# Kernel optimization log

Measured on AMD Instinct MI355X. Metric: run time of the kernel, lower is better.

## Reference

```python
import jax, jax.numpy as jnp
import numpy as np

TOP_K = 2

def setup_inputs() -> dict:
    key = jax.random.key(0)
    k0, k1, k2 = jax.random.split(key, 3)
    N, D, E = 32768, 1024, 8  # tokens, in_dim, expert_num
    x = jax.random.normal(k0, (N, D), dtype=jnp.float32)
    W1 = jax.random.normal(k1, (D // 2, D), dtype=jnp.float32) * (1.0 / np.sqrt(D))
    b1 = jnp.zeros((D // 2,), dtype=jnp.float32)
    W2 = jax.random.normal(k2, (E, D // 2), dtype=jnp.float32) * (1.0 / np.sqrt(D // 2))
    b2 = jnp.zeros((E,), dtype=jnp.float32)
    return {"x": x, "W1": W1, "b1": b1, "W2": W2, "b2": b2}

def reference(x, W1, b1, W2, b2):
    E = W2.shape[0]
    # gate: two stacked Linears (no nonlinearity between, as in source)
    h = x @ W1.T + b1                      # [N, D/2]
    router_logits = h @ W2.T + b2          # [N, E]
    router_probs = jax.nn.softmax(router_logits, axis=-1)
    router_weights, top_k_indices = jax.lax.top_k(router_probs, TOP_K)  # [N, K]
    router_weights = router_weights / jnp.sum(router_weights, axis=-1, keepdims=True)
    expert_masks = jax.nn.one_hot(top_k_indices, E, dtype=jnp.int32)   # [N, K, E]
    expert_masks = jnp.transpose(expert_masks, (2, 1, 0))              # [E, K, N]
    return (router_logits, router_weights, top_k_indices, expert_masks)
```

## Files before the change

kernel.cpp:

```cpp
#include <hip/hip_runtime.h>
#include <math.h>


#define N_TOK 32768
#define D_IN  1024
#define D_H   512
#define N_EXP 8

#define BM      128
#define BK      16
#define THREADS 512
#define NKT     (D_IN / BK)
#define WSLOTS  (NKT * 1024)

typedef _Float16 f16;
typedef __attribute__((ext_vector_type(4)))  _Float16 f16x4;
typedef __attribute__((ext_vector_type(8)))  _Float16 f16x8;
typedef __attribute__((ext_vector_type(16))) float    f32x16;

#define MFMA(a, b, c) __builtin_amdgcn_mfma_f32_32x32x16_f16((a), (b), (c), 0, 0, 0)

__global__ void split_w1(const float* __restrict__ W1,
                         f16* __restrict__ wsH, f16* __restrict__ wsL) {
    const int s = blockIdx.x * 256 + threadIdx.x;
    const int kt  = s >> 10;
    const int ctg = (s >> 6) & 15;
    const int l   = s & 63;
    const int n   = ctg * 32 + (l & 31);
    const int k   = kt * BK + (l >> 5) * 8;
    const float* src = &W1[(size_t)n * D_IN + k];
    float4 a0 = *(const float4*)src;
    float4 a1 = *(const float4*)(src + 4);
    f16x8 hi, lo;
#pragma unroll
    for (int j = 0; j < 4; ++j) {
        float v0 = ((const float*)&a0)[j];
        float v1 = ((const float*)&a1)[j];
        _Float16 h0 = (_Float16)v0, h1 = (_Float16)v1;
        hi[j] = h0;     hi[j + 4] = h1;
        lo[j] = (_Float16)(v0 - (float)h0);
        lo[j + 4] = (_Float16)(v1 - (float)h1);
    }
    *(f16x8*)&wsH[(size_t)s * 8] = hi;
    *(f16x8*)&wsL[(size_t)s * 8] = lo;
}

__global__ __launch_bounds__(THREADS, 1)
void moe_router_mfma(const float* __restrict__ x,
                     const f16* __restrict__ wH,
                     const f16* __restrict__ wL,
                     const float* __restrict__ b1,
                     const float* __restrict__ W2,
                     const float* __restrict__ b2,
                     float* __restrict__ out)
{
    __shared__ __align__(16) f16   AS[2 * 2 * 2048];
    __shared__ __align__(16) float h_s[32 * 512];
    __shared__ __align__(16) float W2s[N_EXP * D_H];
    __shared__ __align__(16) float b1s[D_H];
    __shared__ float b2s[N_EXP];

    const int t    = threadIdx.x;
    const int w    = t >> 6;
    const int lane = t & 63;
    const int m0   = blockIdx.x * BM;

    f32x16 a0c0 = {}, a0c1 = {}, a1c0 = {}, a1c1 = {};
    f32x16 a2c0 = {}, a2c1 = {}, a3c0 = {}, a3c1 = {};

    const int fA   = t >> 1;
    const int qA   = t & 1;
    const int rowA = (fA >> 6) * 32 + (fA & 31);
    const int kA   = ((fA >> 5) & 1) * 8 + qA * 4;
    const float* xsrc = x + (size_t)(m0 + rowA) * D_IN + kA;
    const int aDst = fA * 8 + qA * 4;

    const size_t bOff0 = (size_t)(2 * w + 0) * 512 + (size_t)lane * 8;
    const size_t bOff1 = (size_t)(2 * w + 1) * 512 + (size_t)lane * 8;

    auto stageAwrite = [&](const float4& xv, int buf) {
        f16x4 hi, lo;
        float v[4] = {xv.x, xv.y, xv.z, xv.w};
#pragma unroll
        for (int j = 0; j < 4; ++j) {
            _Float16 h = (_Float16)v[j];
            hi[j] = h;
            lo[j] = (_Float16)(v[j] - (float)h);
        }
        *(f16x4*)&AS[(buf * 2 + 0) * 2048 + aDst] = hi;
        *(f16x4*)&AS[(buf * 2 + 1) * 2048 + aDst] = lo;
    };

    f16x8 Bh0A = *(const f16x8*)(wH + bOff0);
    f16x8 Bh1A = *(const f16x8*)(wH + bOff1);
    f16x8 Bl0A = *(const f16x8*)(wL + bOff0);
    f16x8 Bl1A = *(const f16x8*)(wL + bOff1);
    f16x8 Bh0B, Bh1B, Bl0B, Bl1B;
    {
        float4 xv = *(const float4*)xsrc;
        stageAwrite(xv, 0);
    }
    __syncthreads();

#define BODY(BUF, KT, BH0, BH1, BL0, BL1, NH0, NH1, NL0, NL1) do {             \
        float4 xnxt = {0.f, 0.f, 0.f, 0.f};                                    \
        if ((KT) + 1 < NKT) {                                                  \
            const size_t nb = (size_t)((KT) + 1) * 8192;                       \
            NH0 = *(const f16x8*)(wH + nb + bOff0);                            \
            NH1 = *(const f16x8*)(wH + nb + bOff1);                            \
            NL0 = *(const f16x8*)(wL + nb + bOff0);                            \
            NL1 = *(const f16x8*)(wL + nb + bOff1);                            \
            xnxt = *(const float4*)(xsrc + (size_t)((KT) + 1) * BK);           \
        }                                                                      \
        const f16* ah = &AS[((BUF) * 2 + 0) * 2048];                           \
        const f16* al = &AS[((BUF) * 2 + 1) * 2048];                           \
        f16x8 ah0 = *(const f16x8*)&ah[(0 * 64 + lane) * 8];                   \
        f16x8 al0 = *(const f16x8*)&al[(0 * 64 + lane) * 8];                   \
        f16x8 ah1 = *(const f16x8*)&ah[(1 * 64 + lane) * 8];                   \
        f16x8 al1 = *(const f16x8*)&al[(1 * 64 + lane) * 8];                   \
        f16x8 ah2 = *(const f16x8*)&ah[(2 * 64 + lane) * 8];                   \
        f16x8 al2 = *(const f16x8*)&al[(2 * 64 + lane) * 8];                   \
        f16x8 ah3 = *(const f16x8*)&ah[(3 * 64 + lane) * 8];                   \
        f16x8 al3 = *(const f16x8*)&al[(3 * 64 + lane) * 8];                   \
        __builtin_amdgcn_s_setprio(1);                                         \
        a0c0 = MFMA(ah0, BH0, a0c0); a0c0 = MFMA(al0, BH0, a0c0);              \
        a0c0 = MFMA(ah0, BL0, a0c0);                                           \
        a1c0 = MFMA(ah1, BH0, a1c0); a1c0 = MFMA(al1, BH0, a1c0);              \
        a1c0 = MFMA(ah1, BL0, a1c0);                                           \
        a2c0 = MFMA(ah2, BH0, a2c0); a2c0 = MFMA(al2, BH0, a2c0);              \
        a2c0 = MFMA(ah2, BL0, a2c0);                                           \
        a3c0 = MFMA(ah3, BH0, a3c0); a3c0 = MFMA(al3, BH0, a3c0);              \
        a3c0 = MFMA(ah3, BL0, a3c0);                                           \
        __builtin_amdgcn_s_setprio(0);                                         \
        __builtin_amdgcn_s_barrier();                                          \
        __builtin_amdgcn_s_setprio(1);                                         \
        a0c1 = MFMA(ah0, BH1, a0c1); a0c1 = MFMA(al0, BH1, a0c1);              \
        a0c1 = MFMA(ah0, BL1, a0c1);                                           \
        a1c1 = MFMA(ah1, BH1, a1c1); a1c1 = MFMA(al1, BH1, a1c1);              \
        a1c1 = MFMA(ah1, BL1, a1c1);                                           \
        a2c1 = MFMA(ah2, BH1, a2c1); a2c1 = MFMA(al2, BH1, a2c1);              \
        a2c1 = MFMA(ah2, BL1, a2c1);                                           \
        a3c1 = MFMA(ah3, BH1, a3c1); a3c1 = MFMA(al3, BH1, a3c1);              \
        a3c1 = MFMA(ah3, BL1, a3c1);                                           \
        __builtin_amdgcn_s_setprio(0);                                         \
        if ((KT) + 1 < NKT) stageAwrite(xnxt, (BUF) ^ 1);                      \
        __syncthreads();                                                       \
    } while (0)

    for (int kt = 0; kt < NKT; kt += 2) {
        BODY(0, kt,     Bh0A, Bh1A, Bl0A, Bl1A, Bh0B, Bh1B, Bl0B, Bl1B);
        BODY(1, kt + 1, Bh0B, Bh1B, Bl0B, Bl1B, Bh0A, Bh1A, Bl0A, Bl1A);
    }
#undef BODY

    ((float4*)W2s)[t * 2]     = ((const float4*)W2)[t * 2];
    ((float4*)W2s)[t * 2 + 1] = ((const float4*)W2)[t * 2 + 1];
    if (t < D_H / 4) ((float4*)b1s)[t] = ((const float4*)b1)[t];
    if (t < N_EXP) b2s[t] = b2[t];
    __syncthreads();

    const int n0  = w * 64 + (lane & 31);
    const int n1  = n0 + 32;
    const float bn0 = b1s[n0];
    const float bn1 = b1s[n1];

    float* out_logits = out;
    float* out_w      = out + (size_t)N_TOK * N_EXP;
    float* out_i      = out_w + (size_t)N_TOK * 2;
    float* out_m      = out_i + (size_t)N_TOK * 2;

    auto reduce_rows = [&](int rt) {
#pragma unroll
        for (int rr2 = 0; rr2 < 4; ++rr2) {
            const int rl   = w * 4 + rr2;
            const int grow = m0 + rt * 32 + rl;
            float4 ha = *(const float4*)&h_s[rl * 512 + lane * 4];
            float4 hb = *(const float4*)&h_s[rl * 512 + 256 + lane * 4];
            float v1 = -3.4e38f, v2 = -3.4e38f;
            int   i1 = 0, i2 = 0;
            float pls[8];
#pragma unroll
            for (int e = 0; e < N_EXP; ++e) {
                float4 wa = *(const float4*)&W2s[e * D_H + lane * 4];
                float4 wb = *(const float4*)&W2s[e * D_H + 256 + lane * 4];
                float s = ha.x * wa.x;
                s = fmaf(ha.y, wa.y, s);
                s = fmaf(ha.z, wa.z, s);
                s = fmaf(ha.w, wa.w, s);
                s = fmaf(hb.x, wb.x, s);
                s = fmaf(hb.y, wb.y, s);
                s = fmaf(hb.z, wb.z, s);
                s = fmaf(hb.w, wb.w, s);
#pragma unroll
                for (int off = 1; off < 64; off <<= 1)
                    s += __shfl_xor(s, off);
                s += b2s[e];
                pls[e] = s;
                if (s > v1)      { v2 = v1; i2 = i1; v1 = s; i1 = e; }
                else if (s > v2) { v2 = s;  i2 = e; }
            }
            const float rr   = expf(v2 - v1);
            const float wden = 1.f / (1.f + rr);
            if (lane == 0) {
                float4 lo4 = {pls[0], pls[1], pls[2], pls[3]};
                float4 hi4 = {pls[4], pls[5], pls[6], pls[7]};
                *(float4*)&out_logits[(size_t)grow * N_EXP]     = lo4;
                *(float4*)&out_logits[(size_t)grow * N_EXP + 4] = hi4;
                float2 wv = {wden, rr * wden};
                *(float2*)&out_w[(size_t)grow * 2] = wv;
                float2 iv = {(float)i1, (float)i2};
                *(float2*)&out_i[(size_t)grow * 2] = iv;
            }
            if (lane < 16) {
                const int e   = lane >> 1;
                const int kk  = lane & 1;
                const int sel = kk ? i2 : i1;
                out_m[((size_t)(e * 2 + kk)) * N_TOK + grow] = (sel == e) ? 1.0f : 0.0f;
            }
        }
    };

#define DO_GROUP(AC0, AC1, RT) do {                                            \
        _Pragma("unroll")                                                      \
        for (int rr = 0; rr < 16; ++rr) {                                      \
            const int rl = (rr & 3) + 8 * (rr >> 2) + 4 * (lane >> 5);         \
            h_s[rl * 512 + n0] = AC0[rr] + bn0;                                \
            h_s[rl * 512 + n1] = AC1[rr] + bn1;                                \
        }                                                                      \
        __syncthreads();                                                       \
        reduce_rows(RT);                                                       \
        __syncthreads();                                                       \
    } while (0)

    DO_GROUP(a0c0, a0c1, 0);
    DO_GROUP(a1c0, a1c1, 1);
    DO_GROUP(a2c0, a2c1, 2);
    DO_GROUP(a3c0, a3c1, 3);
#undef DO_GROUP
}

extern "C" void kernel_launch(void* const* d_in, const int* in_sizes, int n_in,
                              void* d_out, int out_size, void* d_ws, size_t ws_size,
                              hipStream_t stream) {
    const float* x  = (const float*)d_in[0];
    const float* W1 = (const float*)d_in[1];
    const float* b1 = (const float*)d_in[2];
    const float* W2 = (const float*)d_in[3];
    const float* b2 = (const float*)d_in[4];
    float* out = (float*)d_out;

    f16* wsH = (f16*)d_ws;
    f16* wsL = wsH + (size_t)WSLOTS * 8;

    split_w1<<<WSLOTS / 256, 256, 0, stream>>>(W1, wsH, wsL);
    moe_router_mfma<<<N_TOK / BM, THREADS, 0, stream>>>(x, wsH, wsL, b1, W2, b2, out);
}
```

Baseline: 130.6 us.

## Double K-step per barrier, interleave MFMA order, alias LDS buffers

```diff
diff --git a/kernel.cpp b/kernel.cpp
--- a/kernel.cpp
+++ b/kernel.cpp
@@ -8,10 +8,9 @@
 #define N_EXP 8
 
 #define BM      128
-#define BK      16
 #define THREADS 512
-#define NKT     (D_IN / BK)
-#define WSLOTS  (NKT * 1024)
+#define NKT2    32
+#define WSLOTS  (64 * 1024)
 
 typedef _Float16 f16;
 typedef __attribute__((ext_vector_type(4)))  _Float16 f16x4;
@@ -27,7 +26,7 @@
     const int ctg = (s >> 6) & 15;
     const int l   = s & 63;
     const int n   = ctg * 32 + (l & 31);
-    const int k   = kt * BK + (l >> 5) * 8;
+    const int k   = kt * 16 + (l >> 5) * 8;
     const float* src = &W1[(size_t)n * D_IN + k];
     float4 a0 = *(const float4*)src;
     float4 a1 = *(const float4*)(src + 4);
@@ -54,11 +53,13 @@
                      const float* __restrict__ b2,
                      float* __restrict__ out)
 {
-    __shared__ __align__(16) f16   AS[2 * 2 * 2048];
-    __shared__ __align__(16) float h_s[32 * 512];
+    __shared__ __align__(16) unsigned char SMEM[65536];
     __shared__ __align__(16) float W2s[N_EXP * D_H];
     __shared__ __align__(16) float b1s[D_H];
     __shared__ float b2s[N_EXP];
+
+    f16*   AS  = (f16*)SMEM;
+    float* h_s = (float*)SMEM;
 
     const int t    = threadIdx.x;
     const int w    = t >> 6;
@@ -72,13 +73,17 @@
     const int qA   = t & 1;
     const int rowA = (fA >> 6) * 32 + (fA & 31);
     const int kA   = ((fA >> 5) & 1) * 8 + qA * 4;
-    const float* xsrc = x + (size_t)(m0 + rowA) * D_IN + kA;
+    const unsigned xOff = (unsigned)(m0 + rowA) * D_IN + kA;
     const int aDst = fA * 8 + qA * 4;
 
-    const size_t bOff0 = (size_t)(2 * w + 0) * 512 + (size_t)lane * 8;
-    const size_t bOff1 = (size_t)(2 * w + 1) * 512 + (size_t)lane * 8;
-
-    auto stageAwrite = [&](const float4& xv, int buf) {
+    const unsigned bO0 = (unsigned)(2 * w + 0) * 512 + (unsigned)lane * 8;
+    const unsigned bO1 = bO0 + 512;
+    const int aO0 = ((0 * 64) + lane) * 8;
+    const int aO1 = ((1 * 64) + lane) * 8;
+    const int aO2 = ((2 * 64) + lane) * 8;
+    const int aO3 = ((3 * 64) + lane) * 8;
+
+    auto stageAwrite = [&](const float4& xv, int buf, int sub) {
         f16x4 hi, lo;
         float v[4] = {xv.x, xv.y, xv.z, xv.w};
 #pragma unroll
@@ -87,69 +92,130 @@
             hi[j] = h;
             lo[j] = (_Float16)(v[j] - (float)h);
         }
-        *(f16x4*)&AS[(buf * 2 + 0) * 2048 + aDst] = hi;
-        *(f16x4*)&AS[(buf * 2 + 1) * 2048 + aDst] = lo;
+        *(f16x4*)&AS[(buf * 2 + 0) * 4096 + sub * 2048 + aDst] = hi;
+        *(f16x4*)&AS[(buf * 2 + 1) * 4096 + sub * 2048 + aDst] = lo;
     };
 
-    f16x8 Bh0A = *(const f16x8*)(wH + bOff0);
-    f16x8 Bh1A = *(const f16x8*)(wH + bOff1);
-    f16x8 Bl0A = *(const f16x8*)(wL + bOff0);
-    f16x8 Bl1A = *(const f16x8*)(wL + bOff1);
-    f16x8 Bh0B, Bh1B, Bl0B, Bl1B;
-    {
-        float4 xv = *(const float4*)xsrc;
-        stageAwrite(xv, 0);
-    }
+    stageAwrite(*(const float4*)(x + xOff), 0, 0);
+    stageAwrite(*(const float4*)(x + (xOff + 16u)), 0, 1);
+    f16x8 AH00 = *(const f16x8*)(wH + bO0);
+    f16x8 AH01 = *(const f16x8*)(wH + bO1);
+    f16x8 AH10 = *(const f16x8*)(wH + (8192u + bO0));
+    f16x8 AH11 = *(const f16x8*)(wH + (8192u + bO1));
+    f16x8 AL00 = *(const f16x8*)(wL + bO0);
+    f16x8 AL01 = *(const f16x8*)(wL + bO1);
+    f16x8 AL10 = *(const f16x8*)(wL + (8192u + bO0));
+    f16x8 AL11 = *(const f16x8*)(wL + (8192u + bO1));
+    f16x8 BH00, BH01, BH10, BH11, BL00, BL01, BL10, BL11;
     __syncthreads();
 
-#define BODY(BUF, KT, BH0, BH1, BL0, BL1, NH0, NH1, NL0, NL1) do {             \
-        float4 xnxt = {0.f, 0.f, 0.f, 0.f};                                    \
-        if ((KT) + 1 < NKT) {                                                  \
-            const size_t nb = (size_t)((KT) + 1) * 8192;                       \
-            NH0 = *(const f16x8*)(wH + nb + bOff0);                            \
-            NH1 = *(const f16x8*)(wH + nb + bOff1);                            \
-            NL0 = *(const f16x8*)(wL + nb + bOff0);                            \
-            NL1 = *(const f16x8*)(wL + nb + bOff1);                            \
-            xnxt = *(const float4*)(xsrc + (size_t)((KT) + 1) * BK);           \
-        }                                                                      \
-        const f16* ah = &AS[((BUF) * 2 + 0) * 2048];                           \
-        const f16* al = &AS[((BUF) * 2 + 1) * 2048];                           \
-        f16x8 ah0 = *(const f16x8*)&ah[(0 * 64 + lane) * 8];                   \
-        f16x8 al0 = *(const f16x8*)&al[(0 * 64 + lane) * 8];                   \
-        f16x8 ah1 = *(const f16x8*)&ah[(1 * 64 + lane) * 8];                   \
-        f16x8 al1 = *(const f16x8*)&al[(1 * 64 + lane) * 8];                   \
-        f16x8 ah2 = *(const f16x8*)&ah[(2 * 64 + lane) * 8];                   \
-        f16x8 al2 = *(const f16x8*)&al[(2 * 64 + lane) * 8];                   \
-        f16x8 ah3 = *(const f16x8*)&ah[(3 * 64 + lane) * 8];                   \
-        f16x8 al3 = *(const f16x8*)&al[(3 * 64 + lane) * 8];                   \
-        __builtin_amdgcn_s_setprio(1);                                         \
-        a0c0 = MFMA(ah0, BH0, a0c0); a0c0 = MFMA(al0, BH0, a0c0);              \
-        a0c0 = MFMA(ah0, BL0, a0c0);                                           \
-        a1c0 = MFMA(ah1, BH0, a1c0); a1c0 = MFMA(al1, BH0, a1c0);              \
-        a1c0 = MFMA(ah1, BL0, a1c0);                                           \
-        a2c0 = MFMA(ah2, BH0, a2c0); a2c0 = MFMA(al2, BH0, a2c0);              \
-        a2c0 = MFMA(ah2, BL0, a2c0);                                           \
-        a3c0 = MFMA(ah3, BH0, a3c0); a3c0 = MFMA(al3, BH0, a3c0);              \
-        a3c0 = MFMA(ah3, BL0, a3c0);                                           \
-        __builtin_amdgcn_s_setprio(0);                                         \
-        __builtin_amdgcn_s_barrier();                                          \
-        __builtin_amdgcn_s_setprio(1);                                         \
-        a0c1 = MFMA(ah0, BH1, a0c1); a0c1 = MFMA(al0, BH1, a0c1);              \
-        a0c1 = MFMA(ah0, BL1, a0c1);                                           \
-        a1c1 = MFMA(ah1, BH1, a1c1); a1c1 = MFMA(al1, BH1, a1c1);              \
-        a1c1 = MFMA(ah1, BL1, a1c1);                                           \
-        a2c1 = MFMA(ah2, BH1, a2c1); a2c1 = MFMA(al2, BH1, a2c1);              \
-        a2c1 = MFMA(ah2, BL1, a2c1);                                           \
-        a3c1 = MFMA(ah3, BH1, a3c1); a3c1 = MFMA(al3, BH1, a3c1);              \
-        a3c1 = MFMA(ah3, BL1, a3c1);                                           \
-        __builtin_amdgcn_s_setprio(0);                                         \
-        if ((KT) + 1 < NKT) stageAwrite(xnxt, (BUF) ^ 1);                      \
+#define BODY(BUF, KTT, CH00, CH01, CH10, CH11, CL00, CL01, CL10, CL11,         \
+                       NH00, NH01, NH10, NH11, NL00, NL01, NL10, NL11)         \
+    do {                                                                       \
+        float4 xn0 = {0.f, 0.f, 0.f, 0.f}, xn1 = {0.f, 0.f, 0.f, 0.f};         \
+        const bool more = (KTT) + 1 < NKT2;                                    \
+        if (more) {                                                            \
+            const unsigned nk = (unsigned)(2 * (KTT) + 2) * 8192u;             \
+            NH00 = *(const f16x8*)(wH + (nk + bO0));                           \
+            NH01 = *(const f16x8*)(wH + (nk + bO1));                           \
+            NH10 = *(const f16x8*)(wH + (nk + 8192u + bO0));                   \
+            NH11 = *(const f16x8*)(wH + (nk + 8192u + bO1));                   \
+            xn0 = *(const float4*)(x + (xOff + (unsigned)((KTT) + 1) * 32u));  \
+            xn1 = *(const float4*)(x + (xOff + (unsigned)((KTT) + 1) * 32u + 16u)); \
+        }                                                                      \
+        const int hiP = ((BUF) * 2 + 0) * 4096;                                \
+        const int loP = ((BUF) * 2 + 1) * 4096;                                \
+        {                                                 \
+            f16x8 ah0 = *(const f16x8*)&AS[hiP + aO0];                         \
+            f16x8 ah1 = *(const f16x8*)&AS[hiP + aO1];                         \
+            f16x8 ah2 = *(const f16x8*)&AS[hiP + aO2];                         \
+            f16x8 ah3 = *(const f16x8*)&AS[hiP + aO3];                         \
+            f16x8 al0 = *(const f16x8*)&AS[loP + aO0];                         \
+            f16x8 al1 = *(const f16x8*)&AS[loP + aO1];                         \
+            f16x8 al2 = *(const f16x8*)&AS[loP + aO2];                         \
+            f16x8 al3 = *(const f16x8*)&AS[loP + aO3];                         \
+            __builtin_amdgcn_s_setprio(1);                                     \
+            a0c0 = MFMA(ah0, CH00, a0c0);                                      \
+            a1c0 = MFMA(ah1, CH00, a1c0);                                      \
+            a2c0 = MFMA(ah2, CH00, a2c0);                                      \
+            a3c0 = MFMA(ah3, CH00, a3c0);                                      \
+            a0c1 = MFMA(ah0, CH01, a0c1);                                      \
+            a1c1 = MFMA(ah1, CH01, a1c1);                                      \
+            a2c1 = MFMA(ah2, CH01, a2c1);                                      \
+            a3c1 = MFMA(ah3, CH01, a3c1);                                      \
+            a0c0 = MFMA(al0, CH00, a0c0);                                      \
+            a1c0 = MFMA(al1, CH00, a1c0);                                      \
+            a2c0 = MFMA(al2, CH00, a2c0);                                      \
+            a3c0 = MFMA(al3, CH00, a3c0);                                      \
+            a0c1 = MFMA(al0, CH01, a0c1);                                      \
+            a1c1 = MFMA(al1, CH01, a1c1);                                      \
+            a2c1 = MFMA(al2, CH01, a2c1);                                      \
+            a3c1 = MFMA(al3, CH01, a3c1);                                      \
+            a0c0 = MFMA(ah0, CL00, a0c0);                                      \
+            a1c0 = MFMA(ah1, CL00, a1c0);                                      \
+            a2c0 = MFMA(ah2, CL00, a2c0);                                      \
+            a3c0 = MFMA(ah3, CL00, a3c0);                                      \
+            a0c1 = MFMA(ah0, CL01, a0c1);                                      \
+            a1c1 = MFMA(ah1, CL01, a1c1);                                      \
+            a2c1 = MFMA(ah2, CL01, a2c1);                                      \
+            a3c1 = MFMA(ah3, CL01, a3c1);                                      \
+            __builtin_amdgcn_s_setprio(0);                                     \
+        }                                                                      \
+        if (more) {    \
+            const unsigned nk = (unsigned)(2 * (KTT) + 2) * 8192u;             \
+            NL00 = *(const f16x8*)(wL + (nk + bO0));                           \
+            NL01 = *(const f16x8*)(wL + (nk + bO1));                           \
+            NL10 = *(const f16x8*)(wL + (nk + 8192u + bO0));                   \
+            NL11 = *(const f16x8*)(wL + (nk + 8192u + bO1));                   \
+        }                                                                      \
+        {                                                 \
+            f16x8 ah0 = *(const f16x8*)&AS[hiP + 2048 + aO0];                  \
+            f16x8 ah1 = *(const f16x8*)&AS[hiP + 2048 + aO1];                  \
+            f16x8 ah2 = *(const f16x8*)&AS[hiP + 2048 + aO2];                  \
+            f16x8 ah3 = *(const f16x8*)&AS[hiP + 2048 + aO3];                  \
+            f16x8 al0 = *(const f16x8*)&AS[loP + 2048 + aO0];                  \
+            f16x8 al1 = *(const f16x8*)&AS[loP + 2048 + aO1];                  \
+            f16x8 al2 = *(const f16x8*)&AS[loP + 2048 + aO2];                  \
+            f16x8 al3 = *(const f16x8*)&AS[loP + 2048 + aO3];                  \
+            __builtin_amdgcn_s_setprio(1);                                     \
+            a0c0 = MFMA(ah0, CH10, a0c0);                                      \
+            a1c0 = MFMA(ah1, CH10, a1c0);                                      \
+            a2c0 = MFMA(ah2, CH10, a2c0);                                      \
+            a3c0 = MFMA(ah3, CH10, a3c0);                                      \
+            a0c1 = MFMA(ah0, CH11, a0c1);                                      \
+            a1c1 = MFMA(ah1, CH11, a1c1);                                      \
+            a2c1 = MFMA(ah2, CH11, a2c1);                                      \
+            a3c1 = MFMA(ah3, CH11, a3c1);                                      \
+            a0c0 = MFMA(al0, CH10, a0c0);                                      \
+            a1c0 = MFMA(al1, CH10, a1c0);                                      \
+            a2c0 = MFMA(al2, CH10, a2c0);                                      \
+            a3c0 = MFMA(al3, CH10, a3c0);                                      \
+            a0c1 = MFMA(al0, CH11, a0c1);                                      \
+            a1c1 = MFMA(al1, CH11, a1c1);                                      \
+            a2c1 = MFMA(al2, CH11, a2c1);                                      \
+            a3c1 = MFMA(al3, CH11, a3c1);                                      \
+            a0c0 = MFMA(ah0, CL10, a0c0);                                      \
+            a1c0 = MFMA(ah1, CL10, a1c0);                                      \
+            a2c0 = MFMA(ah2, CL10, a2c0);                                      \
+            a3c0 = MFMA(ah3, CL10, a3c0);                                      \
+            a0c1 = MFMA(ah0, CL11, a0c1);                                      \
+            a1c1 = MFMA(ah1, CL11, a1c1);                                      \
+            a2c1 = MFMA(ah2, CL11, a2c1);                                      \
+            a3c1 = MFMA(ah3, CL11, a3c1);                                      \
+            __builtin_amdgcn_s_setprio(0);                                     \
+        }                                                                      \
+        if (more) {                                                            \
+            stageAwrite(xn0, (BUF) ^ 1, 0);                                    \
+            stageAwrite(xn1, (BUF) ^ 1, 1);                                    \
+        }                                                                      \
         __syncthreads();                                                       \
     } while (0)
 
-    for (int kt = 0; kt < NKT; kt += 2) {
-        BODY(0, kt,     Bh0A, Bh1A, Bl0A, Bl1A, Bh0B, Bh1B, Bl0B, Bl1B);
-        BODY(1, kt + 1, Bh0B, Bh1B, Bl0B, Bl1B, Bh0A, Bh1A, Bl0A, Bl1A);
+    for (int ktt = 0; ktt < NKT2; ktt += 2) {
+        BODY(0, ktt,     AH00, AH01, AH10, AH11, AL00, AL01, AL10, AL11,
+                         BH00, BH01, BH10, BH11, BL00, BL01, BL10, BL11);
+        BODY(1, ktt + 1, BH00, BH01, BH10, BH11, BL00, BL01, BL10, BL11,
+                         AH00, AH01, AH10, AH11, AL00, AL01, AL10, AL11);
     }
 #undef BODY
 
```

New measurement: 142.2 us. 8.9% more time.
